# Performance work log

Measured on AMD Instinct MI355X. Metric: run time of the kernel, lower is better.

## Reference

```python
import jax, jax.numpy as jnp
import numpy as np

B, S, D, H, MLP = 8, 1024, 768, 12, 3072
HD = D // H
EPS = 1e-5


def setup_inputs() -> dict:
    key = jax.random.key(0)
    ks = jax.random.split(key, 5)
    sd = lambda fan_in: 1.0 / np.sqrt(fan_in)
    return {
        "x": jax.random.normal(ks[0], (B, S, D), jnp.float32),
        "w_qkv": jax.random.normal(ks[1], (D, 3 * D), jnp.float32) * sd(D),
        "w_out": jax.random.normal(ks[2], (D, D), jnp.float32) * sd(D),
        "b_out": jnp.zeros((D,), jnp.float32),
        "w1": jax.random.normal(ks[3], (D, MLP), jnp.float32) * sd(D),
        "b1": jnp.zeros((MLP,), jnp.float32),
        "w2": jax.random.normal(ks[4], (MLP, D), jnp.float32) * sd(MLP),
        "b2": jnp.zeros((D,), jnp.float32),
    }


def _instance_norm(x):
    # torch InstanceNorm2d on a 3D [B,S,D] tensor treats it as unbatched (C,H,W):
    # normalize over (S, D) per batch element, biased var, eps=1e-5, no affine.
    mu = jnp.mean(x, axis=(1, 2), keepdims=True)
    var = jnp.mean(jnp.square(x - mu), axis=(1, 2), keepdims=True)
    return (x - mu) * jax.lax.rsqrt(var + EPS)


def reference(x, w_qkv, w_out, b_out, w1, b1, w2, b2):
    scale = HD ** -0.5
    # --- self-attention branch ---
    h = _instance_norm(x)
    qkv = (h @ w_qkv).reshape(B, S, 3, H, HD)          # (qkv, heads, head_dim) split
    qkv = qkv.transpose(2, 0, 3, 1, 4)                  # [3, B, H, S, HD]
    q, k, v = qkv[0], qkv[1], qkv[2]
    att = jax.nn.softmax(jnp.einsum('bhxd,bhyd->bhxy', q, k) * scale, axis=-1)
    o = jnp.einsum('bhxy,bhyd->bhxd', att, v)           # [B, H, S, HD]
    o = o.transpose(0, 2, 1, 3).reshape(B, S, D)        # b h l d -> b l (h d)
    x = x + (o @ w_out + b_out)
    # --- MLP branch (exact erf GELU, as nn.GELU default) ---
    h2 = _instance_norm(x)
    m = jax.nn.gelu(h2 @ w1 + b1, approximate=False) @ w2 + b2
    return x + m
```

## Files before the change

kernel.cpp:

```cpp
#include <hip/hip_runtime.h>
#include <hip/hip_bf16.h>

typedef __hip_bfloat16 bf16;
typedef __attribute__((ext_vector_type(8))) short short8;
typedef __attribute__((ext_vector_type(4))) float f32x4;

#define B_   8
#define S_   1024
#define D_   768
#define H_   12
#define HD_  64
#define MLP_ 3072
#define SD_  (S_ * D_)

#define QSCALE 0.18033688011112042f

__device__ __forceinline__ void gl2lds16(const bf16* g, bf16* l) {
  __builtin_amdgcn_global_load_lds(
      (const __attribute__((address_space(1))) unsigned*)(const void*)g,
      (__attribute__((address_space(3))) unsigned*)(void*)l, 16, 0, 0);
}

__global__ __launch_bounds__(256) void transpose_all(
    const float* __restrict__ w_qkv, const float* __restrict__ w_out,
    const float* __restrict__ w1, const float* __restrict__ w2,
    bf16* __restrict__ t_qkv, bf16* __restrict__ t_out,
    bf16* __restrict__ t1, bf16* __restrict__ t2,
    float* __restrict__ cs1) {
  const int t = blockIdx.x;
  if (t >= 6912) {
    const int n = (t - 6912) * 256 + threadIdx.x;
    float s = 0.f;
    for (int k0 = 0; k0 < 768; k0 += 8) {
#pragma unroll
      for (int u = 0; u < 8; ++u) s += w1[(long)(k0 + u) * 3072 + n];
    }
    cs1[n] = s;
    return;
  }
  const float* in; bf16* out; int R, C, idx;
  if (t < 1728)      { in = w_qkv; out = t_qkv; R = 768;  C = 2304; idx = t; }
  else if (t < 2304) { in = w_out; out = t_out; R = 768;  C = 768;  idx = t - 1728; }
  else if (t < 4608) { in = w1;    out = t1;    R = 768;  C = 3072; idx = t - 2304; }
  else               { in = w2;    out = t2;    R = 3072; C = 768;  idx = t - 4608; }
  const int nbx = C >> 5;
  const int bx = (idx % nbx) * 32, by = (idx / nbx) * 32;
  __shared__ float tt[32][33];
  const int tx = threadIdx.x & 31, ty = threadIdx.x >> 5;
#pragma unroll
  for (int rr = 0; rr < 32; rr += 8)
    tt[ty + rr][tx] = in[(long)(by + ty + rr) * C + bx + tx];
  __syncthreads();
#pragma unroll
  for (int rr = 0; rr < 32; rr += 8)
    out[(long)(bx + ty + rr) * R + by + tx] = __float2bfloat16(tt[tx][ty + rr]);
}

__global__ __launch_bounds__(256) void stats_partial(const float* __restrict__ x,
                                                     float* __restrict__ redp) {
  const long off = (long)blockIdx.x * 8192;
  float s = 0.f, s2 = 0.f;
#pragma unroll
  for (int it = 0; it < 8; ++it) {
    float4 v = *(const float4*)(x + off + ((long)threadIdx.x + it * 256) * 4);
    s += v.x + v.y + v.z + v.w;
    s2 += v.x * v.x + v.y * v.y + v.z * v.z + v.w * v.w;
  }
#pragma unroll
  for (int o = 1; o < 64; o <<= 1) { s += __shfl_xor(s, o, 64); s2 += __shfl_xor(s2, o, 64); }
  __shared__ float sh[8];
  const int wave = threadIdx.x >> 6, lane = threadIdx.x & 63;
  if (lane == 0) { sh[wave * 2] = s; sh[wave * 2 + 1] = s2; }
  __syncthreads();
  if (threadIdx.x == 0) {
    redp[blockIdx.x * 2]     = sh[0] + sh[2] + sh[4] + sh[6];
    redp[blockIdx.x * 2 + 1] = sh[1] + sh[3] + sh[5] + sh[7];
  }
}

__global__ __launch_bounds__(512) void stats_final(const float* __restrict__ redp,
                                                   float* __restrict__ red_x,
                                                   float* __restrict__ red2) {
  const int b = threadIdx.x >> 6, lane = threadIdx.x & 63;
  const int i0 = (b * 96 + lane) * 2;
  float s  = redp[i0]     + ((lane < 32) ? redp[i0 + 128]     : 0.f);
  float s2 = redp[i0 + 1] + ((lane < 32) ? redp[i0 + 128 + 1] : 0.f);
#pragma unroll
  for (int o = 1; o < 64; o <<= 1) { s += __shfl_xor(s, o, 64); s2 += __shfl_xor(s2, o, 64); }
  if (lane == 0) { red_x[b * 2] = s; red_x[b * 2 + 1] = s2; }
  if (threadIdx.x < 16) red2[threadIdx.x] = 0.f;
}

__global__ __launch_bounds__(256) void norm_k(const float* __restrict__ x,
                                              const float* __restrict__ sums,
                                              bf16* __restrict__ h) {
  const long i = ((long)blockIdx.x * 256 + threadIdx.x) * 8;
  const int b = (int)(i / SD_);
  const float mu = sums[b * 2] * (1.0f / SD_);
  const float var = sums[b * 2 + 1] * (1.0f / SD_) - mu * mu;
  const float rs = rsqrtf(var + 1e-5f);
  float4 v0 = *(const float4*)(x + i);
  float4 v1 = *(const float4*)(x + i + 4);
  __align__(16) bf16 tmp[8];
  tmp[0] = __float2bfloat16((v0.x - mu) * rs);
  tmp[1] = __float2bfloat16((v0.y - mu) * rs);
  tmp[2] = __float2bfloat16((v0.z - mu) * rs);
  tmp[3] = __float2bfloat16((v0.w - mu) * rs);
  tmp[4] = __float2bfloat16((v1.x - mu) * rs);
  tmp[5] = __float2bfloat16((v1.y - mu) * rs);
  tmp[6] = __float2bfloat16((v1.z - mu) * rs);
  tmp[7] = __float2bfloat16((v1.w - mu) * rs);
  *(short8*)(h + i) = *(const short8*)tmp;
}

template <int EPI, bool STATS>
__global__ __launch_bounds__(256) void gemm_k(
    const bf16* __restrict__ A, const bf16* __restrict__ Bt,
    int M, int N, int K,
    const float* __restrict__ biasf, const float* __restrict__ resf,
    const float* __restrict__ cs, const float* __restrict__ stat_in,
    float* __restrict__ outf,
    bf16* __restrict__ outb0, bf16* __restrict__ outb1, bf16* __restrict__ outb2,
    float* __restrict__ statp) {
  __shared__ __align__(16) bf16 As[2][128 * 64];
  __shared__ __align__(16) bf16 Bs[2][64 * 64];
  __shared__ float sred[8];
  const int tid = threadIdx.x;
  const int bm = blockIdx.x * 128, bn = blockIdx.y * 64;
  const int wave = tid >> 6, lane = tid & 63;
  const int quad = lane >> 4, l16 = lane & 15;
  const int wm = (wave >> 1) * 64, wn = (wave & 1) * 32;
  const int swz = l16 & 7;

  f32x4 acc[4][2];
#pragma unroll
  for (int i = 0; i < 4; ++i)
#pragma unroll
    for (int j = 0; j < 2; ++j) acc[i][j] = (f32x4){0.f, 0.f, 0.f, 0.f};

  const int srow = tid >> 3;
  const int sgc = (tid & 7) ^ (srow & 7);
  const bf16* Ab = A + (long)(bm + srow) * K + sgc * 8;
  const bf16* Bb = Bt + (long)(bn + srow) * K + sgc * 8;

  auto stage = [&](int buf, int k0) {
#pragma unroll
    for (int s = 0; s < 4; ++s)
      gl2lds16(Ab + (long)(s * 32) * K + k0, &As[buf][0] + s * 2048 + tid * 8);
#pragma unroll
    for (int s = 0; s < 2; ++s)
      gl2lds16(Bb + (long)(s * 32) * K + k0, &Bs[buf][0] + s * 2048 + tid * 8);
  };

  stage(0, 0);
  const int nk = K >> 6;
  for (int kt = 0; kt < nk; ++kt) {
    const int cur = kt & 1;
    __syncthreads();
    if (kt + 1 < nk) stage(cur ^ 1, (kt + 1) * 64);
    short8 a[2][4], b[2][2];
#pragma unroll
    for (int kk = 0; kk < 2; ++kk) {
      const int co = ((kk * 4 + quad) ^ swz) * 8;
#pragma unroll
      for (int i = 0; i < 4; ++i)
        a[kk][i] = *(const short8*)(&As[cur][0] + (wm + i * 16 + l16) * 64 + co);
#pragma unroll
      for (int j = 0; j < 2; ++j)
        b[kk][j] = *(const short8*)(&Bs[cur][0] + (wn + j * 16 + l16) * 64 + co);
    }
#pragma unroll
    for (int kk = 0; kk < 2; ++kk)
#pragma unroll
      for (int i = 0; i < 4; ++i)
#pragma unroll
        for (int j = 0; j < 2; ++j)
          acc[i][j] = __builtin_amdgcn_mfma_f32_16x16x32_bf16(a[kk][i], b[kk][j], acc[i][j], 0, 0, 0);
  }

  const int m0 = bm + wm + quad * 4;
  const int n0 = bn + wn + l16;
  const int batch = bm >> 10;
  float mu = 0.f, rs = 0.f;
  if (EPI == 2) {
    const float s1 = stat_in[batch * 2], s2v = stat_in[batch * 2 + 1];
    mu = s1 * (1.0f / SD_);
    rs = rsqrtf(s2v * (1.0f / SD_) - mu * mu + 1e-5f);
  }
  float ts = 0.f, ts2 = 0.f;
#pragma unroll
  for (int i = 0; i < 4; ++i) {
#pragma unroll
    for (int j = 0; j < 2; ++j) {
      const int n = n0 + j * 16;
#pragma unroll
      for (int r = 0; r < 4; ++r) {
        const int m = m0 + i * 16 + r;
        float v = acc[i][j][r];
        if (EPI == 0) {
          const int t = n / D_;
          const int rr2 = n - t * D_;
          const int hh = rr2 >> 6, dd = rr2 & 63;
          const int bb = m >> 10, ss = m & 1023;
          const long hoff = (long)(bb * H_ + hh);
          if (t == 0)      outb0[(hoff * S_ + ss) * HD_ + dd] = __float2bfloat16(v * QSCALE);
          else if (t == 1) outb1[(hoff * S_ + ss) * HD_ + dd] = __float2bfloat16(v);
          else             outb2[(hoff * HD_ + dd) * S_ + ss] = __float2bfloat16(v);
        } else if (EPI == 1) {
          v += biasf[n] + resf[(long)m * N + n];
          outf[(long)m * N + n] = v;
          outb0[(long)m * N + n] = __float2bfloat16(v);
          if (STATS) { ts += v; ts2 += v * v; }
        } else if (EPI == 2) {
          v = rs * (v - mu * cs[n]) + biasf[n];
          float u = v * v;
          float y = v * (1.0f + 0.044715f * u) * 0.7978845608028654f;
          float z = exp2f(y * -2.885390081777927f);
          v = v * __builtin_amdgcn_rcpf(1.0f + z);
          outb0[(long)m * N + n] = __float2bfloat16(v);
        } else {
          v += biasf[n] + resf[(long)m * N + n];
          outf[(long)m * N + n] = v;
        }
      }
    }
  }
  if (STATS) {
#pragma unroll
    for (int o = 1; o < 64; o <<= 1) { ts += __shfl_xor(ts, o, 64); ts2 += __shfl_xor(ts2, o, 64); }
    if (lane == 0) { sred[wave * 2] = ts; sred[wave * 2 + 1] = ts2; }
    __syncthreads();
    if (tid == 0) {
      atomicAdd(&statp[batch * 2], sred[0] + sred[2] + sred[4] + sred[6]);
      atomicAdd(&statp[batch * 2 + 1], sred[1] + sred[3] + sred[5] + sred[7]);
    }
  }
}

__global__ __launch_bounds__(256) void attn64(const bf16* __restrict__ q,
                                              const bf16* __restrict__ k,
                                              const bf16* __restrict__ vt,
                                              bf16* __restrict__ o) {
  __shared__ __align__(16) bf16 Ks[2][64 * 64];
  __shared__ __align__(16) bf16 Vs[2][64 * 64];
  __shared__ __align__(16) bf16 Ps[4 * 16 * 64];
  const int bh = blockIdx.x, qt = blockIdx.y;
  const int tid = threadIdx.x, wave = tid >> 6, lane = tid & 63;
  const int quad = lane >> 4, l16 = lane & 15;
  const int sw = (l16 & 7) ^ ((l16 >> 3) & 1);
  const long base = (long)bh * (S_ * HD_);
  const bf16* kg = k + base;
  const bf16* vg = vt + base;

  const int srow = tid >> 3;
  const int scg = (tid & 7) ^ (srow & 7) ^ ((srow >> 3) & 1);

  short8 aq[2];
#pragma unroll
  for (int kk = 0; kk < 2; ++kk)
    aq[kk] = *(const short8*)(q + base + (long)(qt * 64 + wave * 16 + l16) * HD_ +
                              kk * 32 + quad * 8);

  gl2lds16(kg + (long)srow * HD_ + scg * 8, &Ks[0][0] + tid * 8);
  gl2lds16(kg + (long)(32 + srow) * HD_ + scg * 8, &Ks[0][0] + 2048 + tid * 8);
  gl2lds16(vg + (long)srow * S_ + scg * 8, &Vs[0][0] + tid * 8);
  gl2lds16(vg + (long)(32 + srow) * S_ + scg * 8, &Vs[0][0] + 2048 + tid * 8);

  f32x4 oacc[4];
#pragma unroll
  for (int j = 0; j < 4; ++j) oacc[j] = (f32x4){0.f, 0.f, 0.f, 0.f};
  float lp[4] = {0.f, 0.f, 0.f, 0.f};

  for (int c = 0; c < 16; ++c) {
    const int cur = c & 1;
    __syncthreads();

    f32x4 s[4];
#pragma unroll
    for (int nj = 0; nj < 4; ++nj) s[nj] = (f32x4){0.f, 0.f, 0.f, 0.f};
#pragma unroll
    for (int kk = 0; kk < 2; ++kk) {
#pragma unroll
      for (int nj = 0; nj < 4; ++nj) {
        short8 bk = *(const short8*)(&Ks[cur][0] + (nj * 16 + l16) * 64 +
                                     (((kk * 4 + quad) ^ sw) * 8));
        s[nj] = __builtin_amdgcn_mfma_f32_16x16x32_bf16(aq[kk], bk, s[nj], 0, 0, 0);
      }
    }

    if (c < 15) {
      const int nxt = cur ^ 1;
      gl2lds16(kg + (long)((c + 1) * 64 + srow) * HD_ + scg * 8, &Ks[nxt][0] + tid * 8);
      gl2lds16(kg + (long)((c + 1) * 64 + 32 + srow) * HD_ + scg * 8, &Ks[nxt][0] + 2048 + tid * 8);
      gl2lds16(vg + (long)srow * S_ + (c + 1) * 64 + scg * 8, &Vs[nxt][0] + tid * 8);
      gl2lds16(vg + (long)(32 + srow) * S_ + (c + 1) * 64 + scg * 8, &Vs[nxt][0] + 2048 + tid * 8);
    }

#pragma unroll
    for (int r = 0; r < 4; ++r) {
      const int row = quad * 4 + r;
      const int swp = (row & 7) ^ ((row >> 3) & 1);
#pragma unroll
      for (int nj = 0; nj < 4; ++nj) {
        float p = exp2f(s[nj][r]);
        lp[r] += p;
        const int chunk = nj * 2 + (l16 >> 3);
        Ps[wave * 1024 + row * 64 + ((chunk ^ swp) * 8) + (l16 & 7)] =
            __float2bfloat16(p);
      }
    }

#pragma unroll
    for (int kk = 0; kk < 2; ++kk) {
      short8 ap = *(const short8*)(Ps + wave * 1024 + l16 * 64 +
                                   (((kk * 4 + quad) ^ sw) * 8));
#pragma unroll
      for (int dj = 0; dj < 4; ++dj) {
        short8 bv = *(const short8*)(&Vs[cur][0] + (dj * 16 + l16) * 64 +
                                     (((kk * 4 + quad) ^ sw) * 8));
        oacc[dj] = __builtin_amdgcn_mfma_f32_16x16x32_bf16(ap, bv, oacc[dj], 0, 0, 0);
      }
    }
  }

  const int b = bh / H_, hh = bh - b * H_;
#pragma unroll
  for (int r = 0; r < 4; ++r) {
    float l = lp[r];
#pragma unroll
    for (int off = 1; off < 16; off <<= 1) l += __shfl_xor(l, off, 64);
    const int sg = qt * 64 + wave * 16 + quad * 4 + r;
    const float inv = 1.0f / l;
    const long rowoff = ((long)b * S_ + sg) * D_ + hh * HD_;
#pragma unroll
    for (int dj = 0; dj < 4; ++dj)
      o[rowoff + dj * 16 + l16] = __float2bfloat16(oacc[dj][r] * inv);
  }
}

extern "C" void kernel_launch(void* const* d_in, const int* in_sizes, int n_in,
                              void* d_out, int out_size, void* d_ws, size_t ws_size,
                              hipStream_t stream) {
  const float* x     = (const float*)d_in[0];
  const float* w_qkv = (const float*)d_in[1];
  const float* w_out = (const float*)d_in[2];
  const float* b_out = (const float*)d_in[3];
  const float* w1    = (const float*)d_in[4];
  const float* b1    = (const float*)d_in[5];
  const float* w2    = (const float*)d_in[6];
  const float* b2    = (const float*)d_in[7];
  float* out = (float*)d_out;

  bf16* wt_qkv = (bf16*)d_ws;
  bf16* wt_out = wt_qkv + 2304 * 768;
  bf16* wt1    = wt_out + 768 * 768;
  bf16* wt2    = wt1 + 3072 * 768;
  bf16* qb     = wt2 + 768 * 3072;
  bf16* kb     = qb + 6291456;
  bf16* vtb    = kb + 6291456;
  bf16* ob     = vtb + 6291456;
  float* x1f   = (float*)(ob + 6291456);
  bf16* hb     = (bf16*)(x1f + 6291456);
  float* redp  = (float*)(hb + 6291456);
  float* red_x = redp + 1536;
  float* red2  = red_x + 16;
  float* cs1   = red2 + 16;
  bf16* gb     = qb;
  bf16* x1b    = hb;

  transpose_all<<<6924, 256, 0, stream>>>(w_qkv, w_out, w1, w2,
                                          wt_qkv, wt_out, wt1, wt2, cs1);

  stats_partial<<<B_ * 96, 256, 0, stream>>>(x, redp);
  stats_final<<<1, 512, 0, stream>>>(redp, red_x, red2);
  norm_k<<<3072, 256, 0, stream>>>(x, red_x, hb);

  gemm_k<0, false><<<dim3(64, 36), 256, 0, stream>>>(
      hb, wt_qkv, 8192, 2304, 768, nullptr, nullptr, nullptr, nullptr,
      nullptr, qb, kb, vtb, nullptr);
  attn64<<<dim3(B_ * H_, 16), 256, 0, stream>>>(qb, kb, vtb, ob);

  gemm_k<1, true><<<dim3(64, 12), 256, 0, stream>>>(
      ob, wt_out, 8192, 768, 768, b_out, x, nullptr, nullptr,
      x1f, x1b, nullptr, nullptr, red2);

  gemm_k<2, false><<<dim3(64, 48), 256, 0, stream>>>(
      x1b, wt1, 8192, 3072, 768, b1, nullptr, cs1, red2,
      nullptr, gb, nullptr, nullptr, nullptr);

  gemm_k<3, false><<<dim3(64, 12), 256, 0, stream>>>(
      gb, wt2, 8192, 768, 3072, b2, x1f, nullptr, nullptr,
      out, nullptr, nullptr, nullptr, nullptr);
}
```

Before: 401.4 us.

## Transpose QK^T MFMA to pack P stores and move w1 column sums

The QK^T MFMA now has K as the A operand, so each lane holds four consecutive key positions for a single query row. The P tile can then be written to LDS as one packed 8-byte store per sub-tile, and the row sum is kept as a single scalar reduced across quads with shuffles. Separately, the w1 column-sum computation moves out of the transpose kernel, where it used strided fp32 reads, into extra blocks of stats_partial that sum rows of the already-transposed bf16 weights. Because those sums are taken over bf16-rounded values, the correction term changes slightly in precision.

Result: faster. 354.4 us (-11.7%).

```diff
diff --git a/kernel.cpp b/kernel.cpp
--- a/kernel.cpp
+++ b/kernel.cpp
@@ -15,6 +15,12 @@
 
 #define QSCALE 0.18033688011112042f
 
+__device__ __forceinline__ float b2f(short h) {
+  union { unsigned u; float f; } w;
+  w.u = ((unsigned)(unsigned short)h) << 16;
+  return w.f;
+}
+
 __device__ __forceinline__ void gl2lds16(const bf16* g, bf16* l) {
   __builtin_amdgcn_global_load_lds(
       (const __attribute__((address_space(1))) unsigned*)(const void*)g,
@@ -25,19 +31,8 @@
     const float* __restrict__ w_qkv, const float* __restrict__ w_out,
     const float* __restrict__ w1, const float* __restrict__ w2,
     bf16* __restrict__ t_qkv, bf16* __restrict__ t_out,
-    bf16* __restrict__ t1, bf16* __restrict__ t2,
-    float* __restrict__ cs1) {
+    bf16* __restrict__ t1, bf16* __restrict__ t2) {
   const int t = blockIdx.x;
-  if (t >= 6912) {
-    const int n = (t - 6912) * 256 + threadIdx.x;
-    float s = 0.f;
-    for (int k0 = 0; k0 < 768; k0 += 8) {
-#pragma unroll
-      for (int u = 0; u < 8; ++u) s += w1[(long)(k0 + u) * 3072 + n];
-    }
-    cs1[n] = s;
-    return;
-  }
   const float* in; bf16* out; int R, C, idx;
   if (t < 1728)      { in = w_qkv; out = t_qkv; R = 768;  C = 2304; idx = t; }
   else if (t < 2304) { in = w_out; out = t_out; R = 768;  C = 768;  idx = t - 1728; }
@@ -57,7 +52,26 @@
 }
 
 __global__ __launch_bounds__(256) void stats_partial(const float* __restrict__ x,
-                                                     float* __restrict__ redp) {
+                                                     float* __restrict__ redp,
+                                                     const bf16* __restrict__ wt1,
+                                                     float* __restrict__ cs1) {
+  if (blockIdx.x >= 768) {
+    const int bi = blockIdx.x - 768;
+    const int row = bi * 64 + (threadIdx.x >> 2);
+    const int part = threadIdx.x & 3;
+    const bf16* wr = wt1 + (long)row * 768 + part * 192;
+    float s = 0.f;
+#pragma unroll
+    for (int u = 0; u < 24; ++u) {
+      short8 v = *(const short8*)(wr + u * 8);
+#pragma unroll
+      for (int e = 0; e < 8; ++e) s += b2f(v[e]);
+    }
+    s += __shfl_xor(s, 1, 64);
+    s += __shfl_xor(s, 2, 64);
+    if (part == 0) cs1[row] = s;
+    return;
+  }
   const long off = (long)blockIdx.x * 8192;
   float s = 0.f, s2 = 0.f;
 #pragma unroll
@@ -269,7 +283,7 @@
   f32x4 oacc[4];
 #pragma unroll
   for (int j = 0; j < 4; ++j) oacc[j] = (f32x4){0.f, 0.f, 0.f, 0.f};
-  float lp[4] = {0.f, 0.f, 0.f, 0.f};
+  float lp = 0.f;
 
   for (int c = 0; c < 16; ++c) {
     const int cur = c & 1;
@@ -277,14 +291,14 @@
 
     f32x4 s[4];
 #pragma unroll
-    for (int nj = 0; nj < 4; ++nj) s[nj] = (f32x4){0.f, 0.f, 0.f, 0.f};
+    for (int i = 0; i < 4; ++i) s[i] = (f32x4){0.f, 0.f, 0.f, 0.f};
 #pragma unroll
     for (int kk = 0; kk < 2; ++kk) {
 #pragma unroll
-      for (int nj = 0; nj < 4; ++nj) {
-        short8 bk = *(const short8*)(&Ks[cur][0] + (nj * 16 + l16) * 64 +
+      for (int i = 0; i < 4; ++i) {
+        short8 ak = *(const short8*)(&Ks[cur][0] + (i * 16 + l16) * 64 +
                                      (((kk * 4 + quad) ^ sw) * 8));
-        s[nj] = __builtin_amdgcn_mfma_f32_16x16x32_bf16(aq[kk], bk, s[nj], 0, 0, 0);
+        s[i] = __builtin_amdgcn_mfma_f32_16x16x32_bf16(ak, aq[kk], s[i], 0, 0, 0);
       }
     }
 
@@ -297,17 +311,17 @@
     }
 
 #pragma unroll
-    for (int r = 0; r < 4; ++r) {
-      const int row = quad * 4 + r;
-      const int swp = (row & 7) ^ ((row >> 3) & 1);
-#pragma unroll
-      for (int nj = 0; nj < 4; ++nj) {
-        float p = exp2f(s[nj][r]);
-        lp[r] += p;
-        const int chunk = nj * 2 + (l16 >> 3);
-        Ps[wave * 1024 + row * 64 + ((chunk ^ swp) * 8) + (l16 & 7)] =
-            __float2bfloat16(p);
+    for (int i = 0; i < 4; ++i) {
+      __align__(8) bf16 pk[4];
+#pragma unroll
+      for (int r = 0; r < 4; ++r) {
+        float p = exp2f(s[i][r]);
+        lp += p;
+        pk[r] = __float2bfloat16(p);
       }
+      const int chunk = 2 * i + (quad >> 1);
+      *(uint2*)(Ps + wave * 1024 + l16 * 64 + ((chunk ^ sw) * 8) + (quad & 1) * 4) =
+          *(const uint2*)pk;
     }
 
 #pragma unroll
@@ -323,14 +337,15 @@
     }
   }
 
+  float lt = lp;
+  lt += __shfl_xor(lt, 16, 64);
+  lt += __shfl_xor(lt, 32, 64);
+
   const int b = bh / H_, hh = bh - b * H_;
 #pragma unroll
   for (int r = 0; r < 4; ++r) {
-    float l = lp[r];
-#pragma unroll
-    for (int off = 1; off < 16; off <<= 1) l += __shfl_xor(l, off, 64);
+    const float inv = 1.0f / __shfl(lt, quad * 4 + r, 64);
     const int sg = qt * 64 + wave * 16 + quad * 4 + r;
-    const float inv = 1.0f / l;
     const long rowoff = ((long)b * S_ + sg) * D_ + hh * HD_;
 #pragma unroll
     for (int dj = 0; dj < 4; ++dj)
@@ -368,10 +383,10 @@
   bf16* gb     = qb;
   bf16* x1b    = hb;
 
-  transpose_all<<<6924, 256, 0, stream>>>(w_qkv, w_out, w1, w2,
-                                          wt_qkv, wt_out, wt1, wt2, cs1);
-
-  stats_partial<<<B_ * 96, 256, 0, stream>>>(x, redp);
+  transpose_all<<<6912, 256, 0, stream>>>(w_qkv, w_out, w1, w2,
+                                          wt_qkv, wt_out, wt1, wt2);
+
+  stats_partial<<<768 + 48, 256, 0, stream>>>(x, redp, wt1, cs1);
   stats_final<<<1, 512, 0, stream>>>(redp, red_x, red2);
   norm_k<<<3072, 256, 0, stream>>>(x, red_x, hb);
 
```
